# Kernel tuning notes

Hardware: AMD Instinct MI355X
Metric: run time of the kernel (lower is better)

Reference implementation:

```python
import jax, jax.numpy as jnp
import numpy as np

B, L, D_MODEL, N_HEADS = 2, 2048, 2048, 16
HALF = D_MODEL // 2            # 1024
HD = HALF // N_HEADS           # 64 (head dim actually used by the reshape)
SCALE = float(np.sqrt(D_MODEL / N_HEADS))  # sqrt(128), per source's self.scale
EPS = 1e-5


def setup_inputs() -> dict:
    key = jax.random.key(0)
    ks = jax.random.split(key, 12)
    s = 1.0 / np.sqrt(HALF)
    d = dict(
        x_a=jax.random.normal(ks[0], (B, L, HALF), jnp.float32),
        x_b=jax.random.normal(ks[1], (B, L, HALF), jnp.float32),
        Wq_a=jax.random.normal(ks[2], (HALF, HALF), jnp.float32) * s,
        Wq_b=jax.random.normal(ks[3], (HALF, HALF), jnp.float32) * s,
        Wk_a=jax.random.normal(ks[4], (HALF, HALF), jnp.float32) * s,
        Wk_b=jax.random.normal(ks[5], (HALF, HALF), jnp.float32) * s,
        Wv_a=jax.random.normal(ks[6], (HALF, HALF), jnp.float32) * s,
        Wv_b=jax.random.normal(ks[7], (HALF, HALF), jnp.float32) * s,
        Wo_a=jax.random.normal(ks[8], (HALF, HALF), jnp.float32) * s,
        Wo_b=jax.random.normal(ks[9], (HALF, HALF), jnp.float32) * s,
        gamma_a=jnp.ones((HALF,), jnp.float32),
        beta_a=jnp.zeros((HALF,), jnp.float32),
        gamma_b=jnp.ones((HALF,), jnp.float32),
        beta_b=jnp.zeros((HALF,), jnp.float32),
    )
    return d


def _heads(x, W):
    # torch Linear (no bias): x @ W.T, then split heads -> (B, H, L, HD)
    y = jnp.einsum('bld,ed->ble', x, W)
    Bb, Ll, _ = y.shape
    return y.reshape(Bb, Ll, N_HEADS, HD).transpose(0, 2, 1, 3)


def _ln(x, gamma, beta):
    mu = jnp.mean(x, axis=-1, keepdims=True)
    var = jnp.var(x, axis=-1, keepdims=True)
    return (x - mu) * jax.lax.rsqrt(var + EPS) * gamma + beta


def reference(x_a, x_b, Wq_a, Wq_b, Wk_a, Wk_b, Wv_a, Wv_b, Wo_a, Wo_b,
              gamma_a, beta_a, gamma_b, beta_b):
    q_a = _heads(x_a, Wq_a); k_a = _heads(x_a, Wk_a); v_a = _heads(x_a, Wv_a)
    q_b = _heads(x_b, Wq_b); k_b = _heads(x_b, Wk_b); v_b = _heads(x_b, Wv_b)

    # cross-attention: branch a attends over branch b and vice versa
    scores_a = jnp.einsum('bhqd,bhkd->bhqk', q_a, k_b) / SCALE
    scores_b = jnp.einsum('bhqd,bhkd->bhqk', q_b, k_a) / SCALE
    w_a = jax.nn.softmax(scores_a, axis=-1)
    w_b = jax.nn.softmax(scores_b, axis=-1)

    o_a = jnp.einsum('bhqk,bhkd->bhqd', w_a, v_b)
    o_b = jnp.einsum('bhqk,bhkd->bhqd', w_b, v_a)
    o_a = o_a.transpose(0, 2, 1, 3).reshape(x_a.shape)
    o_b = o_b.transpose(0, 2, 1, 3).reshape(x_b.shape)

    o_a = jnp.einsum('bld,ed->ble', o_a, Wo_a)
    o_b = jnp.einsum('bld,ed->ble', o_b, Wo_b)

    y_a = _ln(x_a + o_a, gamma_a, beta_a)
    y_b = _ln(x_b + o_b, gamma_b, beta_b)
    return y_a, y_b
```

## Files before the change

kernel.cpp:

```cpp
#include <hip/hip_runtime.h>
#include <cstdint>
#include <cstddef>

typedef __bf16 bf16x8 __attribute__((ext_vector_type(8)));
typedef float f32x4 __attribute__((ext_vector_type(4)));
typedef unsigned short u16x8 __attribute__((ext_vector_type(8)));
typedef unsigned short u16x4 __attribute__((ext_vector_type(4)));
typedef short s16x4 __attribute__((ext_vector_type(4)));
typedef unsigned short u16;

#define L_SEQ 2048
#define D_HALF 1024
#define HDIM 64
static constexpr float EXP2_SCALE = 0.12751742552639395f;

__device__ inline u16 f2b(float f) {
  uint32_t u; __builtin_memcpy(&u, &f, 4);
  u = u + 0x7FFFu + ((u >> 16) & 1u);
  return (u16)(u >> 16);
}

__device__ inline uint32_t cvt_pk_bf16(float lo, float hi) {
  uint32_t r;
  asm("v_cvt_pk_bf16_f32 %0, %1, %2" : "=v"(r) : "v"(lo), "v"(hi));
  return r;
}

#define GLOAD16(gp, lp) __builtin_amdgcn_global_load_lds( \
    (const __attribute__((address_space(1))) unsigned int*)(gp), \
    (__attribute__((address_space(3))) unsigned int*)(lp), 16, 0, 0)

struct CArgAll { const float* src[10]; u16* dst[10]; };
__global__ __launch_bounds__(256)
void convall(CArgAll a) {
  const int id = blockIdx.x;
  const float* s; u16* d; int blk;
  if (id < 4096) { int p = id >> 11; blk = id & 2047; s = a.src[p]; d = a.dst[p]; }
  else { int w = (id - 4096) >> 9; blk = (id - 4096) & 511; s = a.src[2 + w]; d = a.dst[2 + w]; }
  size_t i = ((size_t)blk * 256 + threadIdx.x) * 8;
  float4 v0 = *(const float4*)(s + i);
  float4 v1 = *(const float4*)(s + i + 4);
  u16x8 p;
  p[0] = f2b(v0.x); p[1] = f2b(v0.y); p[2] = f2b(v0.z); p[3] = f2b(v0.w);
  p[4] = f2b(v1.x); p[5] = f2b(v1.y); p[6] = f2b(v1.z); p[7] = f2b(v1.w);
  *(u16x8*)&d[i] = p;
}

struct GArg { const u16* A; const u16* W; u16* C; const float* R; float* Z;
              int vt; float alpha; };
struct GArgs { GArg g[6]; };

template <bool RESID>
__global__ __launch_bounds__(256)
void gemm_nt(GArgs args, int N, int K) {
  GArg ga = args.g[blockIdx.z];
  __shared__ __attribute__((aligned(16))) u16 As[8192];
  __shared__ __attribute__((aligned(16))) u16 Bs[8192];

  const int tid = threadIdx.x;
  const int wv = tid >> 6, lane = tid & 63;
  const int lane15 = lane & 15, quad = lane >> 4;
  const int m0 = blockIdx.y * 128, n0 = blockIdx.x * 128;
  const int wm = (wv >> 1) * 64, wn = (wv & 1) * 64;

  const int srow = lane >> 3;
  const int scol = ((lane & 7) ^ srow) * 8;

  const u16* pA[4]; const u16* pW[4]; int lo[4];
#pragma unroll
  for (int j = 0; j < 4; j++) {
    int r = wv * 32 + j * 8;
    pA[j] = ga.A + (size_t)(m0 + r + srow) * K + scol;
    pW[j] = ga.W + (size_t)(n0 + r + srow) * K + scol;
    lo[j] = r * 64;
  }

  f32x4 acc[4][4] = {};
  const int swz = (lane15 & 7) << 4;

  for (int k0 = 0; k0 < K; k0 += 64) {
    __syncthreads();
#pragma unroll
    for (int j = 0; j < 4; j++) {
      GLOAD16(pA[j] + k0, &As[lo[j]]);
      GLOAD16(pW[j] + k0, &Bs[lo[j]]);
    }
    __syncthreads();
    const char* ab = (const char*)As;
    const char* bb = (const char*)Bs;
#pragma unroll
    for (int kk = 0; kk < 2; kk++) {
      const int cb = kk * 64 + quad * 16;
      bf16x8 af[4], bw[4];
#pragma unroll
      for (int i = 0; i < 4; i++)
        af[i] = *(const bf16x8*)(ab + (wm + i * 16 + lane15) * 128 + (cb ^ swz));
#pragma unroll
      for (int j = 0; j < 4; j++)
        bw[j] = *(const bf16x8*)(bb + (wn + j * 16 + lane15) * 128 + (cb ^ swz));
#pragma unroll
      for (int i = 0; i < 4; i++)
#pragma unroll
        for (int j = 0; j < 4; j++)
          acc[i][j] = __builtin_amdgcn_mfma_f32_16x16x32_bf16(af[i], bw[j], acc[i][j], 0, 0, 0);
    }
  }

  const float al = ga.alpha;
  if (!RESID && ga.vt) {
#pragma unroll
    for (int i = 0; i < 4; i++)
#pragma unroll
      for (int j = 0; j < 4; j++) {
        int gm0 = m0 + wm + i * 16 + quad * 4;
        int gn  = n0 + wn + j * 16 + lane15;
        int bb2 = gm0 >> 11, tt = gm0 & 2047;
        u16x4 pk;
#pragma unroll
        for (int r = 0; r < 4; r++) pk[r] = f2b(acc[i][j][r] * al);
        *(u16x4*)&ga.C[(size_t)bb2 * 2097152 + (size_t)gn * 2048 + tt] = pk;
      }
  } else {
#pragma unroll
    for (int i = 0; i < 4; i++)
#pragma unroll
      for (int j = 0; j < 4; j++)
#pragma unroll
        for (int r = 0; r < 4; r++) {
          int gm = m0 + wm + i * 16 + quad * 4 + r;
          int gn = n0 + wn + j * 16 + lane15;
          size_t idx = (size_t)gm * N + gn;
          if (RESID) ga.Z[idx] = acc[i][j][r] + ga.R[idx];
          else       ga.C[idx] = f2b(acc[i][j][r] * al);
        }
  }
}

#define SWZ(row, bcol) ((row) * 128 + ((bcol) ^ (((row) & 7) << 4)))

__global__ __launch_bounds__(256, 2)
void attn_kernel(const u16* q_a, const u16* k_a, const u16* vt_a,
                 const u16* q_b, const u16* k_b, const u16* vt_b,
                 u16* o_a, u16* o_b) {
  const int br = blockIdx.z;
  const u16* Q  = br ? q_b : q_a;
  const u16* Kp = br ? k_a : k_b;
  const u16* Vp = br ? vt_a : vt_b;
  u16* O = br ? o_b : o_a;
  const int bh = blockIdx.y;
  const int b = bh >> 4, h = bh & 15;
  const int q0 = blockIdx.x * 128;

  const int tid = threadIdx.x, wv = tid >> 6, lane = tid & 63;
  const int lane15 = lane & 15, quad = lane >> 4;

  __shared__ __attribute__((aligned(16))) u16 Ks[2][4096];
  __shared__ __attribute__((aligned(16))) u16 Vt[2][4096];

  const size_t base   = ((size_t)b * L_SEQ) * D_HALF + (size_t)h * HDIM;
  const size_t vbase  = (size_t)b * 2097152 + (size_t)(h * 64) * 2048;

  const int lrow = lane >> 3;
  const int sc  = ((lane & 7) ^ lrow) * 8;
  const int row0 = wv * 8 + lrow;
  const int row1 = 32 + wv * 8 + lrow;
  const int ldo0 = (wv * 8) * 128;
  const int ldo1 = (32 + wv * 8) * 128;

  bf16x8 qf[2][2];
#pragma unroll
  for (int f = 0; f < 2; f++) {
    const int qrow = q0 + wv * 32 + f * 16 + lane15;
#pragma unroll
    for (int c = 0; c < 2; c++)
      qf[f][c] = *(const bf16x8*)&Q[base + (size_t)qrow * D_HALF + c * 32 + quad * 8];
  }

  GLOAD16(Kp + base + (size_t)row0 * D_HALF + sc, (char*)Ks[0] + ldo0);
  GLOAD16(Kp + base + (size_t)row1 * D_HALF + sc, (char*)Ks[0] + ldo1);
  GLOAD16(Vp + vbase + (size_t)row0 * 2048 + sc,  (char*)Vt[0] + ldo0);
  GLOAD16(Vp + vbase + (size_t)row1 * 2048 + sc,  (char*)Vt[0] + ldo1);
  __syncthreads();

  f32x4 oacc[2][4] = {};
  float lsum[2] = {0.f, 0.f};

  for (int it = 0; it < 32; it++) {
    const int cur = it & 1, nxt = cur ^ 1;
    if (it < 31) {
      const int kt = (it + 1) * 64;
      GLOAD16(Kp + base + (size_t)(kt + row0) * D_HALF + sc, (char*)Ks[nxt] + ldo0);
      GLOAD16(Kp + base + (size_t)(kt + row1) * D_HALF + sc, (char*)Ks[nxt] + ldo1);
      GLOAD16(Vp + vbase + (size_t)row0 * 2048 + kt + sc,    (char*)Vt[nxt] + ldo0);
      GLOAD16(Vp + vbase + (size_t)row1 * 2048 + kt + sc,    (char*)Vt[nxt] + ldo1);
    }

    const char* kb = (const char*)Ks[cur];
    const char* vb = (const char*)Vt[cur];

    f32x4 s[2][4];
    __builtin_amdgcn_s_setprio(1);
#pragma unroll
    for (int nt = 0; nt < 4; nt++) {
      const int krow = nt * 16 + lane15;
      bf16x8 kb0 = *(const bf16x8*)(kb + SWZ(krow, quad * 16));
      bf16x8 kb1 = *(const bf16x8*)(kb + SWZ(krow, 64 + quad * 16));
#pragma unroll
      for (int f = 0; f < 2; f++) {
        f32x4 a0 = {};
        a0 = __builtin_amdgcn_mfma_f32_16x16x32_bf16(kb0, qf[f][0], a0, 0, 0, 0);
        a0 = __builtin_amdgcn_mfma_f32_16x16x32_bf16(kb1, qf[f][1], a0, 0, 0, 0);
        s[f][nt] = a0;
      }
    }
    __builtin_amdgcn_s_setprio(0);

    s16x4 pa[2][4];
#pragma unroll
    for (int f = 0; f < 2; f++)
#pragma unroll
      for (int nt = 0; nt < 4; nt++) {
        float p0 = __builtin_amdgcn_exp2f(s[f][nt][0]);
        float p1 = __builtin_amdgcn_exp2f(s[f][nt][1]);
        float p2 = __builtin_amdgcn_exp2f(s[f][nt][2]);
        float p3 = __builtin_amdgcn_exp2f(s[f][nt][3]);
        lsum[f] += (p0 + p1) + (p2 + p3);
        union { uint32_t u[2]; s16x4 v; } cv;
        cv.u[0] = cvt_pk_bf16(p0, p1);
        cv.u[1] = cvt_pk_bf16(p2, p3);
        pa[f][nt] = cv.v;
      }

    __builtin_amdgcn_s_setprio(1);
#pragma unroll
    for (int dt = 0; dt < 4; dt++) {
      const int vrow = dt * 16 + lane15;
      s16x4 bv[4];
#pragma unroll
      for (int nt = 0; nt < 4; nt++)
        bv[nt] = *(const s16x4*)(vb + SWZ(vrow, nt * 32 + quad * 8));
#pragma unroll
      for (int f = 0; f < 2; f++) {
        f32x4 t = oacc[f][dt];
#pragma unroll
        for (int nt = 0; nt < 4; nt++)
          t = __builtin_amdgcn_mfma_f32_16x16x16bf16_1k(pa[f][nt], bv[nt], t, 0, 0, 0);
        oacc[f][dt] = t;
      }
    }
    __builtin_amdgcn_s_setprio(0);

    __syncthreads();
  }

#pragma unroll
  for (int f = 0; f < 2; f++) {
    float lt = lsum[f];
    lt += __shfl_xor(lt, 16);
    lt += __shfl_xor(lt, 32);
    lsum[f] = lt;
  }
#pragma unroll
  for (int f = 0; f < 2; f++) {
    float linv[4];
#pragma unroll
    for (int r = 0; r < 4; r++)
      linv[r] = 1.0f / __shfl(lsum[f], quad * 4 + r);
#pragma unroll
    for (int dt = 0; dt < 4; dt++)
#pragma unroll
      for (int r = 0; r < 4; r++) {
        float val = oacc[f][dt][r] * linv[r];
        O[base + (size_t)(q0 + wv * 32 + f * 16 + quad * 4 + r) * D_HALF
          + dt * 16 + lane15] = f2b(val);
      }
  }
}

__global__ __launch_bounds__(256)
void ln_kernel(const float* zA, const float* zB,
               const float* gA, const float* bA, const float* gB, const float* bB,
               float* out) {
  const int row = blockIdx.x, br = blockIdx.y;
  const float* z = (br ? zB : zA) + (size_t)row * D_HALF;
  const float* g  = br ? gB : gA;
  const float* be = br ? bB : bA;
  float* o = out + (size_t)br * ((size_t)4096 * D_HALF) + (size_t)row * D_HALF;

  float4 v = ((const float4*)z)[threadIdx.x];
  float s  = v.x + v.y + v.z + v.w;
  float s2 = v.x * v.x + v.y * v.y + v.z * v.z + v.w * v.w;
#pragma unroll
  for (int off = 32; off > 0; off >>= 1) {
    s  += __shfl_down(s, off);
    s2 += __shfl_down(s2, off);
  }
  __shared__ float red[8];
  int w = threadIdx.x >> 6, ln = threadIdx.x & 63;
  if (ln == 0) { red[w] = s; red[4 + w] = s2; }
  __syncthreads();
  if (threadIdx.x == 0) {
    red[0] = red[0] + red[1] + red[2] + red[3];
    red[4] = red[4] + red[5] + red[6] + red[7];
  }
  __syncthreads();
  float mu  = red[0] * (1.0f / 1024.0f);
  float var = red[4] * (1.0f / 1024.0f) - mu * mu;
  float rs  = rsqrtf(fmaxf(var, 0.0f) + 1e-5f);

  int col = threadIdx.x * 4;
  float4 gv = ((const float4*)g)[threadIdx.x];
  float4 bv = ((const float4*)be)[threadIdx.x];
  float4 ov;
  ov.x = (v.x - mu) * rs * gv.x + bv.x;
  ov.y = (v.y - mu) * rs * gv.y + bv.y;
  ov.z = (v.z - mu) * rs * gv.z + bv.z;
  ov.w = (v.w - mu) * rs * gv.w + bv.w;
  *(float4*)&o[col] = ov;
}

extern "C" void kernel_launch(void* const* d_in, const int* in_sizes, int n_in,
                              void* d_out, int out_size, void* d_ws, size_t ws_size,
                              hipStream_t stream) {
  const float* x_a     = (const float*)d_in[0];
  const float* x_b     = (const float*)d_in[1];
  const float* Wq_a    = (const float*)d_in[2];
  const float* Wq_b    = (const float*)d_in[3];
  const float* Wk_a    = (const float*)d_in[4];
  const float* Wk_b    = (const float*)d_in[5];
  const float* Wv_a    = (const float*)d_in[6];
  const float* Wv_b    = (const float*)d_in[7];
  const float* Wo_a    = (const float*)d_in[8];
  const float* Wo_b    = (const float*)d_in[9];
  const float* gamma_a = (const float*)d_in[10];
  const float* beta_a  = (const float*)d_in[11];
  const float* gamma_b = (const float*)d_in[12];
  const float* beta_b  = (const float*)d_in[13];

  const size_t BUF = (size_t)4096 * 1024;
  u16* ws   = (u16*)d_ws;
  u16* q_a  = ws + 0 * BUF; u16* k_a  = ws + 1 * BUF; u16* vt_a = ws + 2 * BUF;
  u16* q_b  = ws + 3 * BUF; u16* k_b  = ws + 4 * BUF; u16* vt_b = ws + 5 * BUF;
  u16* wall = ws + 6 * BUF;
  float* z_a = (float*)(ws + 0 * BUF);
  float* z_b = (float*)(ws + 2 * BUF);

  u16* xbf_a = (u16*)d_out;
  u16* xbf_b = xbf_a + 4194304;
  u16* o_a   = (u16*)d_out;
  u16* o_b   = o_a + 4194304;

  const int N = 1024, K = 1024;

  CArgAll ca;
  ca.src[0] = x_a;  ca.dst[0] = xbf_a;
  ca.src[1] = x_b;  ca.dst[1] = xbf_b;
  ca.src[2] = Wq_a; ca.src[3] = Wk_a; ca.src[4] = Wv_a;
  ca.src[5] = Wq_b; ca.src[6] = Wk_b; ca.src[7] = Wv_b;
  ca.src[8] = Wo_a; ca.src[9] = Wo_b;
  for (int w = 0; w < 8; w++) ca.dst[2 + w] = wall + (size_t)w * 1048576;
  convall<<<dim3(8192), 256, 0, stream>>>(ca);

  GArgs qkv;
  qkv.g[0] = GArg{xbf_a, wall + 0 * 1048576, q_a,  nullptr, nullptr, 0, EXP2_SCALE};
  qkv.g[1] = GArg{xbf_a, wall + 1 * 1048576, k_a,  nullptr, nullptr, 0, 1.0f};
  qkv.g[2] = GArg{xbf_a, wall + 2 * 1048576, vt_a, nullptr, nullptr, 1, 1.0f};
  qkv.g[3] = GArg{xbf_b, wall + 3 * 1048576, q_b,  nullptr, nullptr, 0, EXP2_SCALE};
  qkv.g[4] = GArg{xbf_b, wall + 4 * 1048576, k_b,  nullptr, nullptr, 0, 1.0f};
  qkv.g[5] = GArg{xbf_b, wall + 5 * 1048576, vt_b, nullptr, nullptr, 1, 1.0f};
  gemm_nt<false><<<dim3(8, 32, 6), 256, 0, stream>>>(qkv, N, K);

  attn_kernel<<<dim3(16, 32, 2), 256, 0, stream>>>(q_a, k_a, vt_a, q_b, k_b, vt_b, o_a, o_b);

  GArgs op;
  op.g[0] = GArg{o_a, wall + 6 * 1048576, nullptr, x_a, z_a, 0, 1.0f};
  op.g[1] = GArg{o_b, wall + 7 * 1048576, nullptr, x_b, z_b, 0, 1.0f};
  op.g[2] = op.g[0]; op.g[3] = op.g[0]; op.g[4] = op.g[0]; op.g[5] = op.g[0];
  gemm_nt<true><<<dim3(8, 32, 2), 256, 0, stream>>>(op, N, K);

  ln_kernel<<<dim3(4096, 2), 256, 0, stream>>>(z_a, z_b, gamma_a, beta_a,
                                               gamma_b, beta_b, (float*)d_out);
}
```

Before: 326.1 us.

## Split KV range across two wave groups per attention block and merge via LDS

The attention block grows to 512 threads: two groups of four waves each handle half of the key/value sequence with their own double-buffered K/V tiles, so each group runs 16 iterations instead of 32. Afterwards the second group writes its unnormalized output accumulators and row sums to shared memory, and the first group adds them in, normalizes and stores. This relies on the softmax using no running max, so partial results can simply be added. It doubles LDS use per block, adds an extra barrier and LDS round trip, and the merge scratch (about 35 KB) runs past the end of the K buffer into the adjacent V buffer.

```diff
diff --git a/kernel.cpp b/kernel.cpp
--- a/kernel.cpp
+++ b/kernel.cpp
@@ -138,7 +138,7 @@
 
 #define SWZ(row, bcol) ((row) * 128 + ((bcol) ^ (((row) & 7) << 4)))
 
-__global__ __launch_bounds__(256, 2)
+__global__ __launch_bounds__(512, 2)
 void attn_kernel(const u16* q_a, const u16* k_a, const u16* vt_a,
                  const u16* q_b, const u16* k_b, const u16* vt_b,
                  u16* o_a, u16* o_b) {
@@ -151,11 +151,13 @@
   const int b = bh >> 4, h = bh & 15;
   const int q0 = blockIdx.x * 128;
 
-  const int tid = threadIdx.x, wv = tid >> 6, lane = tid & 63;
+  const int tid = threadIdx.x;
+  const int w = tid >> 6, lane = tid & 63;
+  const int kvh = w >> 2, wv = w & 3;
   const int lane15 = lane & 15, quad = lane >> 4;
 
-  __shared__ __attribute__((aligned(16))) u16 Ks[2][4096];
-  __shared__ __attribute__((aligned(16))) u16 Vt[2][4096];
+  __shared__ __attribute__((aligned(16))) u16 Ks[2][2][4096];
+  __shared__ __attribute__((aligned(16))) u16 Vt[2][2][4096];
 
   const size_t base   = ((size_t)b * L_SEQ) * D_HALF + (size_t)h * HDIM;
   const size_t vbase  = (size_t)b * 2097152 + (size_t)(h * 64) * 2048;
@@ -166,6 +168,7 @@
   const int row1 = 32 + wv * 8 + lrow;
   const int ldo0 = (wv * 8) * 128;
   const int ldo1 = (32 + wv * 8) * 128;
+  const int kbase = kvh * 1024;
 
   bf16x8 qf[2][2];
 #pragma unroll
@@ -176,27 +179,27 @@
       qf[f][c] = *(const bf16x8*)&Q[base + (size_t)qrow * D_HALF + c * 32 + quad * 8];
   }
 
-  GLOAD16(Kp + base + (size_t)row0 * D_HALF + sc, (char*)Ks[0] + ldo0);
-  GLOAD16(Kp + base + (size_t)row1 * D_HALF + sc, (char*)Ks[0] + ldo1);
-  GLOAD16(Vp + vbase + (size_t)row0 * 2048 + sc,  (char*)Vt[0] + ldo0);
-  GLOAD16(Vp + vbase + (size_t)row1 * 2048 + sc,  (char*)Vt[0] + ldo1);
+  GLOAD16(Kp + base + (size_t)(kbase + row0) * D_HALF + sc, (char*)Ks[kvh][0] + ldo0);
+  GLOAD16(Kp + base + (size_t)(kbase + row1) * D_HALF + sc, (char*)Ks[kvh][0] + ldo1);
+  GLOAD16(Vp + vbase + (size_t)row0 * 2048 + kbase + sc,    (char*)Vt[kvh][0] + ldo0);
+  GLOAD16(Vp + vbase + (size_t)row1 * 2048 + kbase + sc,    (char*)Vt[kvh][0] + ldo1);
   __syncthreads();
 
   f32x4 oacc[2][4] = {};
   float lsum[2] = {0.f, 0.f};
 
-  for (int it = 0; it < 32; it++) {
+  for (int it = 0; it < 16; it++) {
     const int cur = it & 1, nxt = cur ^ 1;
-    if (it < 31) {
-      const int kt = (it + 1) * 64;
-      GLOAD16(Kp + base + (size_t)(kt + row0) * D_HALF + sc, (char*)Ks[nxt] + ldo0);
-      GLOAD16(Kp + base + (size_t)(kt + row1) * D_HALF + sc, (char*)Ks[nxt] + ldo1);
-      GLOAD16(Vp + vbase + (size_t)row0 * 2048 + kt + sc,    (char*)Vt[nxt] + ldo0);
-      GLOAD16(Vp + vbase + (size_t)row1 * 2048 + kt + sc,    (char*)Vt[nxt] + ldo1);
-    }
-
-    const char* kb = (const char*)Ks[cur];
-    const char* vb = (const char*)Vt[cur];
+    if (it < 15) {
+      const int kt = kbase + (it + 1) * 64;
+      GLOAD16(Kp + base + (size_t)(kt + row0) * D_HALF + sc, (char*)Ks[kvh][nxt] + ldo0);
+      GLOAD16(Kp + base + (size_t)(kt + row1) * D_HALF + sc, (char*)Ks[kvh][nxt] + ldo1);
+      GLOAD16(Vp + vbase + (size_t)row0 * 2048 + kt + sc,    (char*)Vt[kvh][nxt] + ldo0);
+      GLOAD16(Vp + vbase + (size_t)row1 * 2048 + kt + sc,    (char*)Vt[kvh][nxt] + ldo1);
+    }
+
+    const char* kb = (const char*)Ks[kvh][cur];
+    const char* vb = (const char*)Vt[kvh][cur];
 
     f32x4 s[2][4];
     __builtin_amdgcn_s_setprio(1);
@@ -253,27 +256,49 @@
     __syncthreads();
   }
 
-#pragma unroll
-  for (int f = 0; f < 2; f++) {
-    float lt = lsum[f];
-    lt += __shfl_xor(lt, 16);
-    lt += __shfl_xor(lt, 32);
-    lsum[f] = lt;
-  }
-#pragma unroll
-  for (int f = 0; f < 2; f++) {
-    float linv[4];
-#pragma unroll
-    for (int r = 0; r < 4; r++)
-      linv[r] = 1.0f / __shfl(lsum[f], quad * 4 + r);
-#pragma unroll
-    for (int dt = 0; dt < 4; dt++)
-#pragma unroll
-      for (int r = 0; r < 4; r++) {
-        float val = oacc[f][dt][r] * linv[r];
-        O[base + (size_t)(q0 + wv * 32 + f * 16 + quad * 4 + r) * D_HALF
-          + dt * 16 + lane15] = f2b(val);
-      }
+  float* cb = (float*)&Ks[0][0][0];
+  const int slot = (wv * 64 + lane) * 35;
+  if (kvh == 1) {
+#pragma unroll
+    for (int f = 0; f < 2; f++) {
+#pragma unroll
+      for (int dt = 0; dt < 4; dt++)
+        *(f32x4*)&cb[slot + f * 16 + dt * 4] = oacc[f][dt];
+      cb[slot + 32 + f] = lsum[f];
+    }
+  }
+  __syncthreads();
+  if (kvh == 0) {
+#pragma unroll
+    for (int f = 0; f < 2; f++) {
+#pragma unroll
+      for (int dt = 0; dt < 4; dt++)
+        oacc[f][dt] += *(const f32x4*)&cb[slot + f * 16 + dt * 4];
+      lsum[f] += cb[slot + 32 + f];
+    }
+
+#pragma unroll
+    for (int f = 0; f < 2; f++) {
+      float lt = lsum[f];
+      lt += __shfl_xor(lt, 16);
+      lt += __shfl_xor(lt, 32);
+      lsum[f] = lt;
+    }
+#pragma unroll
+    for (int f = 0; f < 2; f++) {
+      float linv[4];
+#pragma unroll
+      for (int r = 0; r < 4; r++)
+        linv[r] = 1.0f / __shfl(lsum[f], quad * 4 + r);
+#pragma unroll
+      for (int dt = 0; dt < 4; dt++)
+#pragma unroll
+        for (int r = 0; r < 4; r++) {
+          float val = oacc[f][dt][r] * linv[r];
+          O[base + (size_t)(q0 + wv * 32 + f * 16 + quad * 4 + r) * D_HALF
+            + dt * 16 + lane15] = f2b(val);
+        }
+    }
   }
 }
 
@@ -370,7 +395,7 @@
   qkv.g[5] = GArg{xbf_b, wall + 5 * 1048576, vt_b, nullptr, nullptr, 1, 1.0f};
   gemm_nt<false><<<dim3(8, 32, 6), 256, 0, stream>>>(qkv, N, K);
 
-  attn_kernel<<<dim3(16, 32, 2), 256, 0, stream>>>(q_a, k_a, vt_a, q_b, k_b, vt_b, o_a, o_b);
+  attn_kernel<<<dim3(16, 32, 2), 512, 0, stream>>>(q_a, k_a, vt_a, q_b, k_b, vt_b, o_a, o_b);
 
   GArgs op;
   op.g[0] = GArg{o_a, wall + 6 * 1048576, nullptr, x_a, z_a, 0, 1.0f};
```

Measured after the change: 360.8 us. 1.11x slower.
